# Kernel optimization log

Measured on AMD Instinct MI355X. Metric: run time of the kernel, lower is better.

## Reference

```python
import jax, jax.numpy as jnp
import numpy as np
import math

V, D, H, KVH, L, T, B = 32000, 1024, 16, 4, 4, 2048, 2
HD = D // H            # head_dim = 64
GROUP = H // KVH       # GQA group size = 4
KVW = KVH * HD         # kv width = 256
EPS = 1e-5


def _alibi_slopes(n_heads):
    # n_heads=16 is a power of two
    start = 2.0 ** (-2.0 ** (-(math.log2(n_heads) - 3)))
    return np.array([start * start ** i for i in range(n_heads)], dtype=np.float32)


def setup_inputs() -> dict:
    key = jax.random.key(0)
    ks = jax.random.split(key, 8)
    s = 0.02
    inp = {
        "tok_emb": jax.random.normal(ks[0], (V, D), jnp.float32) * s,
        "ln1_s": jnp.ones((L, D), jnp.float32),
        "ln1_b": jnp.zeros((L, D), jnp.float32),
        "qkv_w": jax.random.normal(ks[1], (L, D, D + 2 * KVW), jnp.float32) * s,
        "qkv_b": jnp.zeros((L, D + 2 * KVW), jnp.float32),
        "proj_w": jax.random.normal(ks[2], (L, D, D), jnp.float32) * s,
        "proj_b": jnp.zeros((L, D), jnp.float32),
        "ln2_s": jnp.ones((L, D), jnp.float32),
        "ln2_b": jnp.zeros((L, D), jnp.float32),
        "fc1_w": jax.random.normal(ks[3], (L, D, 4 * D), jnp.float32) * s,
        "fc1_b": jnp.zeros((L, 4 * D), jnp.float32),
        "fc2_w": jax.random.normal(ks[4], (L, 4 * D, D), jnp.float32) * s,
        "fc2_b": jnp.zeros((L, D), jnp.float32),
        "lnf_s": jnp.ones((D,), jnp.float32),
        "lnf_b": jnp.zeros((D,), jnp.float32),
        "idx": jax.random.randint(ks[5], (B, T), 0, V, jnp.int32),
    }
    return inp


def _ln(x, s, b):
    mu = jnp.mean(x, axis=-1, keepdims=True)
    var = jnp.var(x, axis=-1, keepdims=True)
    return (x - mu) * jax.lax.rsqrt(var + EPS) * s + b


def _forward(tok_emb, ln1_s, ln1_b, qkv_w, qkv_b, proj_w, proj_b,
             ln2_s, ln2_b, fc1_w, fc1_b, fc2_w, fc2_b, lnf_s, lnf_b, idx):
    x = tok_emb[idx]  # (B, T, D); ALiBi => no learned positional embedding

    # combined causal mask + ALiBi bias: (1, H, T, T)
    slopes = jnp.asarray(_alibi_slopes(H)).reshape(1, H, 1, 1)
    pos = jnp.arange(T, dtype=jnp.float32)
    rel = jnp.minimum(pos[None, :] - pos[:, None], 0.0)  # (T, T), clamp_max(0)
    causal = pos[None, :] <= pos[:, None]
    bias = jnp.where(causal[None, None], rel[None, None] * slopes, -jnp.inf)

    scale = 1.0 / math.sqrt(HD)
    for l in range(L):
        h = _ln(x, ln1_s[l], ln1_b[l])
        qkv = h @ qkv_w[l] + qkv_b[l]
        q = qkv[..., :D].reshape(B, T, H, HD).transpose(0, 2, 1, 3)
        k = qkv[..., D:D + KVW].reshape(B, T, KVH, HD).transpose(0, 2, 1, 3)
        v = qkv[..., D + KVW:].reshape(B, T, KVH, HD).transpose(0, 2, 1, 3)
        k = jnp.repeat(k, GROUP, axis=1)  # GQA broadcast -> (B, H, T, HD)
        v = jnp.repeat(v, GROUP, axis=1)
        att = jnp.einsum("bhqd,bhkd->bhqk", q, k) * scale + bias
        att = jax.nn.softmax(att, axis=-1)
        o = jnp.einsum("bhqk,bhkd->bhqd", att, v)
        o = o.transpose(0, 2, 1, 3).reshape(B, T, D)
        x = x + o @ proj_w[l] + proj_b[l]
        h = _ln(x, ln2_s[l], ln2_b[l])
        x = x + jax.nn.gelu(h @ fc1_w[l] + fc1_b[l], approximate=False) @ fc2_w[l] + fc2_b[l]

    x = _ln(x, lnf_s, lnf_b)
    logits = x @ tok_emb.T  # tied head (no bias)
    return logits


def reference(tok_emb, ln1_s, ln1_b, qkv_w, qkv_b, proj_w, proj_b,
              ln2_s, ln2_b, fc1_w, fc1_b, fc2_w, fc2_b, lnf_s, lnf_b, idx):
    return _forward(tok_emb, ln1_s, ln1_b, qkv_w, qkv_b, proj_w, proj_b,
                    ln2_s, ln2_b, fc1_w, fc1_b, fc2_w, fc2_b, lnf_s, lnf_b, idx)
```

## Files before the change

### kernel.cpp

```cpp
#include <hip/hip_runtime.h>

#define DEV __device__ __forceinline__
typedef unsigned short u16;
typedef __bf16 bf16_t;
typedef bf16_t bf16x8 __attribute__((ext_vector_type(8)));
typedef float f32x4 __attribute__((ext_vector_type(4)));

DEV u16 f2bf(float f){ unsigned u=__float_as_uint(f); return (u16)((u + 0x7fffu + ((u>>16)&1u))>>16); }

DEV void gl_lds16(const void* g, void* l){
  __builtin_amdgcn_global_load_lds((__attribute__((address_space(1))) void*)g,
                                   (__attribute__((address_space(3))) void*)l, 16, 0, 0);
}
DEV f32x4 MFMA(bf16x8 a, bf16x8 b, f32x4 c){
  return __builtin_amdgcn_mfma_f32_16x16x32_bf16(a, b, c, 0, 0, 0);
}
DEV bf16x8 ld8(const u16* p){ return *(const bf16x8*)p; }

__global__ __launch_bounds__(256) void k_embed(const int* __restrict__ idx,
                                               const float* __restrict__ emb,
                                               float* __restrict__ x){
  int row = blockIdx.x;
  int tok = idx[row];
  const float4* s = (const float4*)(emb + (size_t)tok*1024);
  float4* d = (float4*)(x + (size_t)row*1024);
  d[threadIdx.x] = s[threadIdx.x];
}

__global__ __launch_bounds__(256) void k_ln(const float* __restrict__ x,
                                            const float* __restrict__ sc,
                                            const float* __restrict__ bi,
                                            u16* __restrict__ out){
  int row = blockIdx.x;
  const float* xr = x + (size_t)row*1024;
  float4 v = ((const float4*)xr)[threadIdx.x];
  float s = v.x+v.y+v.z+v.w;
  float q = v.x*v.x+v.y*v.y+v.z*v.z+v.w*v.w;
  #pragma unroll
  for(int m=1;m<64;m<<=1){ s += __shfl_xor(s,m); q += __shfl_xor(q,m); }
  __shared__ float ss[4], sq[4];
  int w = threadIdx.x>>6;
  if((threadIdx.x&63)==0){ ss[w]=s; sq[w]=q; }
  __syncthreads();
  s = ss[0]+ss[1]+ss[2]+ss[3];
  q = sq[0]+sq[1]+sq[2]+sq[3];
  float mu = s*(1.f/1024.f);
  float var = q*(1.f/1024.f) - mu*mu;
  float rs = rsqrtf(var + 1e-5f);
  float4 sv = ((const float4*)sc)[threadIdx.x];
  float4 bv = ((const float4*)bi)[threadIdx.x];
  ushort4 o;
  o.x = f2bf((v.x-mu)*rs*sv.x + bv.x);
  o.y = f2bf((v.y-mu)*rs*sv.y + bv.y);
  o.z = f2bf((v.z-mu)*rs*sv.z + bv.z);
  o.w = f2bf((v.w-mu)*rs*sv.w + bv.w);
  *(ushort4*)(out + (size_t)row*1024 + threadIdx.x*4) = o;
}

__global__ __launch_bounds__(256) void k_convT(const float* __restrict__ W,
                                               u16* __restrict__ Wt, int K, int N){
  __shared__ float tile[32][33];
  int n0 = blockIdx.x*32, k0 = blockIdx.y*32;
  int tx = threadIdx.x & 31, ty = threadIdx.x >> 5;
  #pragma unroll
  for(int i=0;i<4;i++)
    tile[ty + i*8][tx] = W[(size_t)(k0 + ty + i*8)*N + n0 + tx];
  __syncthreads();
  #pragma unroll
  for(int i=0;i<4;i++)
    Wt[(size_t)(n0 + ty + i*8)*K + k0 + tx] = f2bf(tile[tx][ty + i*8]);
}

__global__ __launch_bounds__(256) void k_conv(const float* __restrict__ in,
                                              u16* __restrict__ out, int n4){
  int i = blockIdx.x*256 + threadIdx.x;
  if(i < n4){
    float4 v = ((const float4*)in)[i];
    ushort4 o; o.x=f2bf(v.x); o.y=f2bf(v.y); o.z=f2bf(v.z); o.w=f2bf(v.w);
    ((ushort4*)out)[i] = o;
  }
}

template<int EPI, int SWAP>
__global__ __launch_bounds__(256) void k_gemm(const u16* __restrict__ A,
                                              const u16* __restrict__ Bt,
                                              const float* __restrict__ bias,
                                              void* __restrict__ out,
                                              float* __restrict__ res,
                                              int M, int N, int K, int m_base){
  __shared__ __align__(16) u16 As[128*64];
  __shared__ __align__(16) u16 Bs[128*64];
  int t = threadIdx.x, l = t & 63, w = t >> 6;
  int g = l >> 4, lr = l & 15;
  int wr = w >> 1, wc = w & 1;
  int m0, n0;
  if constexpr(SWAP){ m0 = m_base + blockIdx.x*128; n0 = blockIdx.y*128; }
  else              { m0 = m_base + blockIdx.y*128; n0 = blockIdx.x*128; }
  f32x4 acc[4][4];
  #pragma unroll
  for(int i=0;i<4;i++)
    #pragma unroll
    for(int j=0;j<4;j++) acc[i][j] = f32x4{0.f,0.f,0.f,0.f};

  int sr = t >> 3;
  int sc = (((t & 7) ^ (sr & 7)) * 8);
  const u16* pa = A  + (size_t)(m0 + sr)*K + sc;
  const u16* pb = Bt + (size_t)(n0 + sr)*K + sc;
  u16* lda = As + t*8;
  u16* ldb = Bs + t*8;
  const int rs_a = (lr & 7)*8;

  for(int k0=0; k0<K; k0+=64){
    #pragma unroll
    for(int i=0;i<4;i++){
      gl_lds16(pa + (size_t)(i*32)*K, lda + i*2048);
      gl_lds16(pb + (size_t)(i*32)*K, ldb + i*2048);
    }
    pa += 64; pb += 64;
    __syncthreads();
    bf16x8 af[4][2], bfr[4][2];
    #pragma unroll
    for(int mi=0;mi<4;mi++){
      int row = wr*64 + mi*16 + lr;
      af[mi][0] = ld8(&As[row*64 + ((g*8     ) ^ rs_a)]);
      af[mi][1] = ld8(&As[row*64 + ((g*8 + 32) ^ rs_a)]);
    }
    #pragma unroll
    for(int ni=0;ni<4;ni++){
      int row = wc*64 + ni*16 + lr;
      bfr[ni][0] = ld8(&Bs[row*64 + ((g*8     ) ^ rs_a)]);
      bfr[ni][1] = ld8(&Bs[row*64 + ((g*8 + 32) ^ rs_a)]);
    }
    #pragma unroll
    for(int mi=0;mi<4;mi++)
      #pragma unroll
      for(int ni=0;ni<4;ni++){
        acc[mi][ni] = MFMA(af[mi][0], bfr[ni][0], acc[mi][ni]);
        acc[mi][ni] = MFMA(af[mi][1], bfr[ni][1], acc[mi][ni]);
      }
    __syncthreads();
  }

  float bv[4];
  #pragma unroll
  for(int ni=0;ni<4;ni++){
    if constexpr(EPI==3) bv[ni] = 0.f;
    else bv[ni] = bias[n0 + wc*64 + ni*16 + lr];
  }
  #pragma unroll
  for(int mi=0;mi<4;mi++){
    int row = m0 + wr*64 + mi*16 + g*4;
    #pragma unroll
    for(int ni=0;ni<4;ni++){
      int col = n0 + wc*64 + ni*16 + lr;
      #pragma unroll
      for(int r=0;r<4;r++){
        float v = acc[mi][ni][r] + bv[ni];
        size_t oidx = (size_t)(row + r)*N + col;
        if constexpr(EPI==0){
          ((u16*)out)[oidx] = f2bf(v);
        } else if constexpr(EPI==1){
          res[oidx] += v;
        } else if constexpr(EPI==2){
          float gv = 0.5f*v*(1.f + erff(v*0.70710678118654752f));
          ((u16*)out)[oidx] = f2bf(gv);
        } else {
          ((float*)out)[oidx] = v;
        }
      }
    }
  }
}

__global__ __launch_bounds__(256) void k_gemm_f32b(const u16* __restrict__ A,
                                                   const float* __restrict__ B,
                                                   float* __restrict__ out,
                                                   int M, int N, int K, int m_base){
  __shared__ __align__(16) u16 As[128*32];
  __shared__ __align__(16) u16 Bs[128*32];
  int t = threadIdx.x, l = t & 63, w = t >> 6;
  int g = l >> 4, lr = l & 15;
  int wr = w >> 1, wc = w & 1;
  int m0 = m_base + blockIdx.y*128, n0 = blockIdx.x*128;
  f32x4 acc[4][4];
  #pragma unroll
  for(int i=0;i<4;i++)
    #pragma unroll
    for(int j=0;j<4;j++) acc[i][j] = f32x4{0.f,0.f,0.f,0.f};

  int r0 = t >> 2, c0 = (t & 3)*8;
  const u16* pa0 = A + (size_t)(m0 + r0)*K + c0;
  const u16* pa1 = A + (size_t)(m0 + r0 + 64)*K + c0;
  u16* la0 = As + t*8;  u16* la1 = As + (t+256)*8;
  int br = t >> 1, bc = (t & 1)*16;
  const float* pb = B + (size_t)(n0 + br)*K + bc;

  for(int k0=0; k0<K; k0+=32){
    gl_lds16(pa0, la0); gl_lds16(pa1, la1);
    pa0 += 32; pa1 += 32;
    float4 f0 = ((const float4*)pb)[0];
    float4 f1 = ((const float4*)pb)[1];
    float4 f2 = ((const float4*)pb)[2];
    float4 f3 = ((const float4*)pb)[3];
    pb += 32;
    ushort4 u0{f2bf(f0.x),f2bf(f0.y),f2bf(f0.z),f2bf(f0.w)};
    ushort4 u1{f2bf(f1.x),f2bf(f1.y),f2bf(f1.z),f2bf(f1.w)};
    ushort4 u2{f2bf(f2.x),f2bf(f2.y),f2bf(f2.z),f2bf(f2.w)};
    ushort4 u3{f2bf(f3.x),f2bf(f3.y),f2bf(f3.z),f2bf(f3.w)};
    *(ushort4*)&Bs[br*32 + bc +  0] = u0;
    *(ushort4*)&Bs[br*32 + bc +  4] = u1;
    *(ushort4*)&Bs[br*32 + bc +  8] = u2;
    *(ushort4*)&Bs[br*32 + bc + 12] = u3;
    __syncthreads();
    bf16x8 af[4], bfr[4];
    #pragma unroll
    for(int mi=0;mi<4;mi++) af[mi]  = ld8(&As[(wr*64 + mi*16 + lr)*32 + g*8]);
    #pragma unroll
    for(int ni=0;ni<4;ni++) bfr[ni] = ld8(&Bs[(wc*64 + ni*16 + lr)*32 + g*8]);
    #pragma unroll
    for(int mi=0;mi<4;mi++)
      #pragma unroll
      for(int ni=0;ni<4;ni++)
        acc[mi][ni] = MFMA(af[mi], bfr[ni], acc[mi][ni]);
    __syncthreads();
  }

  #pragma unroll
  for(int mi=0;mi<4;mi++){
    int row = m0 + wr*64 + mi*16 + g*4;
    #pragma unroll
    for(int ni=0;ni<4;ni++){
      int col = n0 + wc*64 + ni*16 + lr;
      #pragma unroll
      for(int r=0;r<4;r++)
        out[(size_t)(row + r)*N + col] = acc[mi][ni][r];
    }
  }
}

__global__ __launch_bounds__(256) void k_attn(const u16* __restrict__ qkv,
                                              u16* __restrict__ atto){
  __shared__ __align__(16) u16 Ksm[64*72];
  __shared__ __align__(16) u16 Vsm[64*72];
  __shared__ __align__(16) u16 Psm[4][16*72];
  int t = threadIdx.x, l = t & 63, w = t >> 6, g = l >> 4, lr = l & 15;
  int bh = blockIdx.y; int b = bh >> 4, h = bh & 15, kvh = h >> 2;
  int qb = blockIdx.x * 64;
  const float L2E = 1.44269504088896f;
  const float C1  = 0.125f * L2E;
  float slopeL = exp2f(-0.5f*(float)(h+1)) * L2E;
  float sLkt[4];
  #pragma unroll
  for(int kt=0;kt<4;kt++) sLkt[kt] = slopeL*(float)(kt*16+lr);

  int qrow = qb + w*16 + lr;
  const u16* qp = qkv + (size_t)(b*2048 + qrow)*1536 + h*64;
  bf16x8 qf0 = ld8(qp + g*8);
  bf16x8 qf1 = ld8(qp + 32 + g*8);

  bf16_t onev = (bf16_t)1.0f;
  bf16x8 onesb = {onev,onev,onev,onev,onev,onev,onev,onev};

  f32x4 oacc[4];
  #pragma unroll
  for(int i=0;i<4;i++) oacc[i] = f32x4{0.f,0.f,0.f,0.f};
  f32x4 lsum = f32x4{0.f,0.f,0.f,0.f};

  int nkb = blockIdx.x + 1;
  for(int kb=0; kb<nkb; kb++){
    __syncthreads();
    #pragma unroll
    for(int i=0;i<2;i++){
      int tt = t + i*256;
      int key = tt >> 3, ho = (tt & 7)*8;
      const u16* src = qkv + (size_t)(b*2048 + kb*64 + key)*1536 + 1024 + kvh*64 + ho;
      *(int4*)&Ksm[key*72 + ho] = *(const int4*)src;
    }
    {
      int key0 = (t>>3)*2, hd0 = (t&7)*8;
      const u16* v0 = qkv + (size_t)(b*2048 + kb*64 + key0)*1536 + 1280 + kvh*64 + hd0;
      int4 A0 = *(const int4*)v0;
      int4 A1 = *(const int4*)(v0 + 1536);
      const u16* ua = (const u16*)&A0; const u16* ub = (const u16*)&A1;
      #pragma unroll
      for(int j=0;j<8;j++){
        unsigned pr = (unsigned)ua[j] | ((unsigned)ub[j]<<16);
        *(unsigned*)&Vsm[(hd0+j)*72 + key0] = pr;
      }
    }
    __syncthreads();
    f32x4 sacc[4];
    #pragma unroll
    for(int kt=0;kt<4;kt++) sacc[kt] = f32x4{0.f,0.f,0.f,0.f};
    #pragma unroll
    for(int kt=0;kt<4;kt++){
      bf16x8 kf0 = ld8(&Ksm[(kt*16+lr)*72 + g*8]);
      bf16x8 kf1 = ld8(&Ksm[(kt*16+lr)*72 + 32 + g*8]);
      sacc[kt] = MFMA(qf0, kf0, sacc[kt]);
      sacc[kt] = MFMA(qf1, kf1, sacc[kt]);
    }
    #pragma unroll
    for(int r=0;r<4;r++){
      int q = qb + w*16 + g*4 + r;
      float base = slopeL*(float)(kb*64 - q) - 8.0f*L2E;
      #pragma unroll
      for(int kt=0;kt<4;kt++){
        int key = kb*64 + kt*16 + lr;
        float f = fmaf(sacc[kt][r], C1, base + sLkt[kt]);
        float p = (key <= q) ? exp2f(f) : 0.f;
        Psm[w][(g*4+r)*72 + kt*16 + lr] = f2bf(p);
      }
    }
    #pragma unroll
    for(int ks=0;ks<2;ks++){
      bf16x8 pf = ld8(&Psm[w][lr*72 + ks*32 + g*8]);
      lsum = MFMA(pf, onesb, lsum);
      #pragma unroll
      for(int ht=0;ht<4;ht++){
        bf16x8 vf = ld8(&Vsm[(ht*16+lr)*72 + ks*32 + g*8]);
        oacc[ht] = MFMA(pf, vf, oacc[ht]);
      }
    }
  }
  #pragma unroll
  for(int ht=0;ht<4;ht++){
    #pragma unroll
    for(int r=0;r<4;r++){
      float o = oacc[ht][r] / lsum[r];
      atto[(size_t)(b*2048 + qb + w*16 + g*4 + r)*1024 + h*64 + ht*16 + lr] = f2bf(o);
    }
  }
}

extern "C" void kernel_launch(void* const* d_in, const int* in_sizes, int n_in,
                              void* d_out, int out_size, void* d_ws, size_t ws_size,
                              hipStream_t stream) {
  const float* tok_emb = (const float*)d_in[0];
  const float* ln1_s   = (const float*)d_in[1];
  const float* ln1_b   = (const float*)d_in[2];
  const float* qkv_w   = (const float*)d_in[3];
  const float* qkv_b   = (const float*)d_in[4];
  const float* proj_w  = (const float*)d_in[5];
  const float* proj_b  = (const float*)d_in[6];
  const float* ln2_s   = (const float*)d_in[7];
  const float* ln2_b   = (const float*)d_in[8];
  const float* fc1_w   = (const float*)d_in[9];
  const float* fc1_b   = (const float*)d_in[10];
  const float* fc2_w   = (const float*)d_in[11];
  const float* fc2_b   = (const float*)d_in[12];
  const float* lnf_s   = (const float*)d_in[13];
  const float* lnf_b   = (const float*)d_in[14];
  const int*   idx     = (const int*)d_in[15];

  char* ob = (char*)d_out;
  float* xf32  = (float*)(ob);
  u16* qkv_bf  = (u16*)(ob + (size_t)16777216);
  u16* atto_bf = (u16*)(ob + (size_t)29360128);
  u16* mid_bf  = (u16*)(ob + (size_t)37748736);
  u16* wt_bf   = (u16*)(ob + (size_t)71303168);
  u16* h_bf    = (u16*)d_ws;
  float* out   = (float*)d_out;

  bool big_ws = ws_size >= (size_t)(8388608 + 65536000);
  u16* te_bf = big_ws ? (u16*)((char*)d_ws + 8388608)
                      : (u16*)(ob + (size_t)83886080);

  k_conv<<<32000, 256, 0, stream>>>(tok_emb, te_bf, 8192000);
  k_embed<<<4096, 256, 0, stream>>>(idx, tok_emb, xf32);

  for(int l=0; l<4; l++){
    k_ln<<<4096, 256, 0, stream>>>(xf32, ln1_s + (size_t)l*1024, ln1_b + (size_t)l*1024, h_bf);
    k_convT<<<dim3(48,32), 256, 0, stream>>>(qkv_w + (size_t)l*1024*1536, wt_bf, 1024, 1536);
    k_gemm<0,0><<<dim3(12,32), 256, 0, stream>>>(h_bf, wt_bf, qkv_b + (size_t)l*1536,
                                                 qkv_bf, nullptr, 4096, 1536, 1024, 0);
    k_attn<<<dim3(32,32), 256, 0, stream>>>(qkv_bf, atto_bf);
    k_convT<<<dim3(32,32), 256, 0, stream>>>(proj_w + (size_t)l*1024*1024, wt_bf, 1024, 1024);
    k_gemm<1,0><<<dim3(8,32), 256, 0, stream>>>(atto_bf, wt_bf, proj_b + (size_t)l*1024,
                                                nullptr, xf32, 4096, 1024, 1024, 0);
    k_ln<<<4096, 256, 0, stream>>>(xf32, ln2_s + (size_t)l*1024, ln2_b + (size_t)l*1024, h_bf);
    k_convT<<<dim3(128,32), 256, 0, stream>>>(fc1_w + (size_t)l*1024*4096, wt_bf, 1024, 4096);
    k_gemm<2,0><<<dim3(32,32), 256, 0, stream>>>(h_bf, wt_bf, fc1_b + (size_t)l*4096,
                                                 mid_bf, nullptr, 4096, 4096, 1024, 0);
    k_convT<<<dim3(32,128), 256, 0, stream>>>(fc2_w + (size_t)l*4096*1024, wt_bf, 4096, 1024);
    k_gemm<1,0><<<dim3(8,32), 256, 0, stream>>>(mid_bf, wt_bf, fc2_b + (size_t)l*1024,
                                                nullptr, xf32, 4096, 1024, 4096, 0);
  }
  k_ln<<<4096, 256, 0, stream>>>(xf32, lnf_s, lnf_b, h_bf);

  if(big_ws){
    k_gemm<3,1><<<dim3(32,250), 256, 0, stream>>>(h_bf, te_bf, nullptr, out, nullptr,
                                                  4096, 32000, 1024, 0);
  } else {
    k_gemm<3,1><<<dim3(5,250), 256, 0, stream>>>(h_bf, te_bf, nullptr, out, nullptr,
                                                 4096, 32000, 1024, 0);
    k_gemm<3,1><<<dim3(22,250), 256, 0, stream>>>(h_bf, te_bf, nullptr, out, nullptr,
                                                  4096, 32000, 1024, 1280);
    k_gemm_f32b<<<dim3(250,5), 256, 0, stream>>>(h_bf, tok_emb, out,
                                                 4096, 32000, 1024, 640);
  }
}
```

Measured before the change: 1.783 ms.

## Batch weight conversion up front, swizzle V tile in LDS, rebalance logits split

All four layers' weights are transposed and converted to bf16 in four batched launches before the layer loop, using a z-grid layer offset, instead of one conversion per GEMM inside the loop. The V tile in shared memory is stored with an XOR swizzle on the column index to reduce LDS bank conflicts on the transposed writes and fragment reads. The extra weight buffers occupy more of the output scratch region, so the fallback location of the bf16 embedding copy moves and the logits GEMM partition across launches changes. This cuts launch count and serialization but uses more scratch memory and depends on the output buffer being large enough for the new offsets.

```diff
diff --git a/kernel.cpp b/kernel.cpp
--- a/kernel.cpp
+++ b/kernel.cpp
@@ -60,6 +60,8 @@
 __global__ __launch_bounds__(256) void k_convT(const float* __restrict__ W,
                                                u16* __restrict__ Wt, int K, int N){
   __shared__ float tile[32][33];
+  size_t loff = (size_t)blockIdx.z * K * N;
+  W  += loff;  Wt += loff;
   int n0 = blockIdx.x*32, k0 = blockIdx.y*32;
   int tx = threadIdx.x & 31, ty = threadIdx.x >> 5;
   #pragma unroll
@@ -284,8 +286,10 @@
       const u16* ua = (const u16*)&A0; const u16* ub = (const u16*)&A1;
       #pragma unroll
       for(int j=0;j<8;j++){
+        int row = hd0 + j;
+        int colp = key0 ^ ((row>>3)*8);
         unsigned pr = (unsigned)ua[j] | ((unsigned)ub[j]<<16);
-        *(unsigned*)&Vsm[(hd0+j)*72 + key0] = pr;
+        *(unsigned*)&Vsm[row*72 + colp] = pr;
       }
     }
     __syncthreads();
@@ -317,7 +321,9 @@
       lsum = MFMA(pf, onesb, lsum);
       #pragma unroll
       for(int ht=0;ht<4;ht++){
-        bf16x8 vf = ld8(&Vsm[(ht*16+lr)*72 + ks*32 + g*8]);
+        int row = ht*16 + lr;
+        int colp = (ks*32 + g*8) ^ ((row>>3)*8);
+        bf16x8 vf = ld8(&Vsm[row*72 + colp]);
         oacc[ht] = MFMA(pf, vf, oacc[ht]);
       }
     }
@@ -357,32 +363,39 @@
   u16* qkv_bf  = (u16*)(ob + (size_t)16777216);
   u16* atto_bf = (u16*)(ob + (size_t)29360128);
   u16* mid_bf  = (u16*)(ob + (size_t)37748736);
-  u16* wt_bf   = (u16*)(ob + (size_t)71303168);
+  u16* wt_qkv  = (u16*)(ob + (size_t)71303168);
+  u16* wt_proj = (u16*)(ob + (size_t)83886080);
+  u16* wt_fc1  = (u16*)(ob + (size_t)92274688);
+  u16* wt_fc2  = (u16*)(ob + (size_t)125829120);
   u16* h_bf    = (u16*)d_ws;
   float* out   = (float*)d_out;
 
   bool big_ws = ws_size >= (size_t)(8388608 + 65536000);
   u16* te_bf = big_ws ? (u16*)((char*)d_ws + 8388608)
-                      : (u16*)(ob + (size_t)83886080);
+                      : (u16*)(ob + (size_t)294912000);
 
   k_conv<<<32000, 256, 0, stream>>>(tok_emb, te_bf, 8192000);
   k_embed<<<4096, 256, 0, stream>>>(idx, tok_emb, xf32);
+  k_convT<<<dim3(48,32,4), 256, 0, stream>>>(qkv_w,  wt_qkv, 1024, 1536);
+  k_convT<<<dim3(32,32,4), 256, 0, stream>>>(proj_w, wt_proj, 1024, 1024);
+  k_convT<<<dim3(128,32,4), 256, 0, stream>>>(fc1_w, wt_fc1, 1024, 4096);
+  k_convT<<<dim3(32,128,4), 256, 0, stream>>>(fc2_w, wt_fc2, 4096, 1024);
 
   for(int l=0; l<4; l++){
     k_ln<<<4096, 256, 0, stream>>>(xf32, ln1_s + (size_t)l*1024, ln1_b + (size_t)l*1024, h_bf);
-    k_convT<<<dim3(48,32), 256, 0, stream>>>(qkv_w + (size_t)l*1024*1536, wt_bf, 1024, 1536);
-    k_gemm<0,0><<<dim3(12,32), 256, 0, stream>>>(h_bf, wt_bf, qkv_b + (size_t)l*1536,
+    k_gemm<0,0><<<dim3(12,32), 256, 0, stream>>>(h_bf, wt_qkv + (size_t)l*1536*1024,
+                                                 qkv_b + (size_t)l*1536,
                                                  qkv_bf, nullptr, 4096, 1536, 1024, 0);
     k_attn<<<dim3(32,32), 256, 0, stream>>>(qkv_bf, atto_bf);
-    k_convT<<<dim3(32,32), 256, 0, stream>>>(proj_w + (size_t)l*1024*1024, wt_bf, 1024, 1024);
-    k_gemm<1,0><<<dim3(8,32), 256, 0, stream>>>(atto_bf, wt_bf, proj_b + (size_t)l*1024,
+    k_gemm<1,0><<<dim3(8,32), 256, 0, stream>>>(atto_bf, wt_proj + (size_t)l*1024*1024,
+                                                proj_b + (size_t)l*1024,
                                                 nullptr, xf32, 4096, 1024, 1024, 0);
     k_ln<<<4096, 256, 0, stream>>>(xf32, ln2_s + (size_t)l*1024, ln2_b + (size_t)l*1024, h_bf);
-    k_convT<<<dim3(128,32), 256, 0, stream>>>(fc1_w + (size_t)l*1024*4096, wt_bf, 1024, 4096);
-    k_gemm<2,0><<<dim3(32,32), 256, 0, stream>>>(h_bf, wt_bf, fc1_b + (size_t)l*4096,
+    k_gemm<2,0><<<dim3(32,32), 256, 0, stream>>>(h_bf, wt_fc1 + (size_t)l*4096*1024,
+                                                 fc1_b + (size_t)l*4096,
                                                  mid_bf, nullptr, 4096, 4096, 1024, 0);
-    k_convT<<<dim3(32,128), 256, 0, stream>>>(fc2_w + (size_t)l*4096*1024, wt_bf, 4096, 1024);
-    k_gemm<1,0><<<dim3(8,32), 256, 0, stream>>>(mid_bf, wt_bf, fc2_b + (size_t)l*1024,
+    k_gemm<1,0><<<dim3(8,32), 256, 0, stream>>>(mid_bf, wt_fc2 + (size_t)l*1024*4096,
+                                                fc2_b + (size_t)l*1024,
                                                 nullptr, xf32, 4096, 1024, 4096, 0);
   }
   k_ln<<<4096, 256, 0, stream>>>(xf32, lnf_s, lnf_b, h_bf);
@@ -391,11 +404,11 @@
     k_gemm<3,1><<<dim3(32,250), 256, 0, stream>>>(h_bf, te_bf, nullptr, out, nullptr,
                                                   4096, 32000, 1024, 0);
   } else {
-    k_gemm<3,1><<<dim3(5,250), 256, 0, stream>>>(h_bf, te_bf, nullptr, out, nullptr,
-                                                 4096, 32000, 1024, 0);
-    k_gemm<3,1><<<dim3(22,250), 256, 0, stream>>>(h_bf, te_bf, nullptr, out, nullptr,
-                                                  4096, 32000, 1024, 1280);
-    k_gemm_f32b<<<dim3(250,5), 256, 0, stream>>>(h_bf, tok_emb, out,
-                                                 4096, 32000, 1024, 640);
-  }
-}
+    k_gemm<3,1><<<dim3(18,250), 256, 0, stream>>>(h_bf, te_bf, nullptr, out, nullptr,
+                                                  4096, 32000, 1024, 0);
+    k_gemm<3,1><<<dim3(10,250), 256, 0, stream>>>(h_bf, te_bf, nullptr, out, nullptr,
+                                                  4096, 32000, 1024, 2816);
+    k_gemm_f32b<<<dim3(250,4), 256, 0, stream>>>(h_bf, tok_emb, out,
+                                                 4096, 32000, 1024, 2304);
+  }
+}
```

After: 1.729 ms. -3.0%, faster.
